# Optimization experiments

Measured on AMD Instinct MI355X. Metric: run time of the kernel, lower is better.

## Reference

```python
import jax, jax.numpy as jnp
import numpy as np

T, B, I, H = 1200, 32, 512, 512


def setup_inputs() -> dict:
    key = jax.random.key(0)
    ks = jax.random.split(key, 10)
    s = 0.1
    x = jax.random.normal(ks[0], (T, B, I), dtype=jnp.float32)
    lengths = jax.random.randint(ks[1], (B,), 1, T + 1)
    lengths = lengths.at[0].set(T)  # ensure padded output length == T (static shape)
    return {
        "x": x,
        "output_lengths": lengths,
        "w_ih_fwd": jax.random.normal(ks[2], (4 * H, I), dtype=jnp.float32) * s,
        "w_hh_fwd": jax.random.normal(ks[3], (4 * H, H), dtype=jnp.float32) * s,
        "b_ih_fwd": jax.random.normal(ks[4], (4 * H,), dtype=jnp.float32) * s,
        "b_hh_fwd": jax.random.normal(ks[5], (4 * H,), dtype=jnp.float32) * s,
        "w_ih_bwd": jax.random.normal(ks[6], (4 * H, I), dtype=jnp.float32) * s,
        "w_hh_bwd": jax.random.normal(ks[7], (4 * H, H), dtype=jnp.float32) * s,
        "b_ih_bwd": jax.random.normal(ks[8], (4 * H,), dtype=jnp.float32) * s,
        "b_hh_bwd": jax.random.normal(ks[9], (4 * H,), dtype=jnp.float32) * s,
    }


def _lstm_dir(x, mask, w_ih, w_hh, b_ih, b_hh):
    """Masked unidirectional LSTM (PyTorch gate order i,f,g,o).
    x: (T,B,I), mask: (T,B,1) bool. Returns outputs (T,B,H), (h_n, c_n)."""
    h0 = jnp.zeros((x.shape[1], w_hh.shape[1]), dtype=x.dtype)
    c0 = jnp.zeros_like(h0)
    # Precompute input projection for all timesteps at once (one big GEMM).
    x_proj = jnp.einsum('tbi,gi->tbg', x, w_ih) + (b_ih + b_hh)

    def step(carry, inp):
        h, c = carry
        xp, m = inp  # xp: (B,4H), m: (B,1)
        gates = xp + h @ w_hh.T
        i, f, g, o = jnp.split(gates, 4, axis=-1)
        i = jax.nn.sigmoid(i)
        f = jax.nn.sigmoid(f)
        g = jnp.tanh(g)
        o = jax.nn.sigmoid(o)
        c_new = f * c + i * g
        h_new = o * jnp.tanh(c_new)
        # Packed semantics: state frozen past each sequence's length.
        h = jnp.where(m, h_new, h)
        c = jnp.where(m, c_new, c)
        out = jnp.where(m, h_new, jnp.zeros_like(h_new))  # pad positions -> 0
        return (h, c), out

    (h_n, c_n), outs = jax.lax.scan(step, (h0, c0), (x_proj, mask))
    return outs, h_n, c_n


def reference(x, output_lengths, w_ih_fwd, w_hh_fwd, b_ih_fwd, b_hh_fwd,
              w_ih_bwd, w_hh_bwd, b_ih_bwd, b_hh_bwd):
    t_idx = jnp.arange(x.shape[0])  # (T,)
    mask = (t_idx[:, None] < output_lengths[None, :])[:, :, None]  # (T,B,1)

    # Forward direction.
    out_f, h_f, c_f = _lstm_dir(x, mask, w_ih_fwd, w_hh_fwd, b_ih_fwd, b_hh_fwd)

    # Backward direction: reverse each sequence within its valid region.
    rev_idx = jnp.clip(output_lengths[None, :] - 1 - t_idx[:, None], 0)  # (T,B)
    x_rev = jnp.take_along_axis(x, rev_idx[:, :, None], axis=0) * mask
    out_r, h_b, c_b = _lstm_dir(x_rev, mask, w_ih_bwd, w_hh_bwd, b_ih_bwd, b_hh_bwd)
    out_b = jnp.take_along_axis(out_r, rev_idx[:, :, None], axis=0) * mask

    # Bidirectional view(...,2,-1).sum(2) == sum of direction outputs.
    out = out_f + out_b
    h_n = jnp.stack([h_f, h_b], axis=0)  # (2,B,H)
    c_n = jnp.stack([c_f, c_b], axis=0)
    return out, h_n, c_n
```

## Files before the change

kernel.cpp:

```cpp
#include <hip/hip_runtime.h>
#include <cstdint>
#include <cstddef>

typedef unsigned short u16;
typedef unsigned int u32;
typedef unsigned long long u64;
typedef short bf16x8 __attribute__((ext_vector_type(8)));
typedef float f32x4 __attribute__((ext_vector_type(4)));
typedef unsigned short u16x4 __attribute__((ext_vector_type(4)));

#define T_LEN 1200

#define O_X     0ull
#define O_WIH   39321600ull
#define O_WHH   43515904ull
#define O_BIAS  47710208ull
#define O_HBUF  47726592ull
#define WS_NEED 47988736ull

#define HO 19660800ull
#define CO 19693568ull

#define HROW 516

__device__ __forceinline__ u16 f2bf(float f) {
  union { float f; unsigned u; } v; v.f = f;
  unsigned r = v.u + 0x7FFFu + ((v.u >> 16) & 1u);
  return (u16)(r >> 16);
}
__device__ __forceinline__ float sigm(float x) { return 1.f / (1.f + __expf(-x)); }
__device__ __forceinline__ float tanh_s(float x) {
  float ax = fabsf(x);
  float e = __expf(-2.f * ax);
  float t = (1.f - e) / (1.f + e);
  return x < 0.f ? -t : t;
}

__device__ __forceinline__ u64 ld_dev64(const u32* p) {
  return __hip_atomic_load((const u64*)p, __ATOMIC_RELAXED, __HIP_MEMORY_SCOPE_AGENT);
}
__device__ __forceinline__ u32 ld_dev32(const u32* p) {
  return __hip_atomic_load(p, __ATOMIC_RELAXED, __HIP_MEMORY_SCOPE_AGENT);
}
__device__ __forceinline__ void st_dev32(u32* p, unsigned v) {
  __hip_atomic_store(p, v, __ATOMIC_RELAXED, __HIP_MEMORY_SCOPE_AGENT);
}

__global__ __launch_bounds__(256) void cast_x_k(const float4* __restrict__ x,
                                                u16* __restrict__ xb) {
  int i = blockIdx.x * 256 + threadIdx.x;
  float4 v = x[i];
  u16x4 o;
  o.x = f2bf(v.x); o.y = f2bf(v.y); o.z = f2bf(v.z); o.w = f2bf(v.w);
  *(u16x4*)(xb + (size_t)i * 4) = o;
}

__global__ __launch_bounds__(256) void prep_w_k(
    const float* __restrict__ wih_f, const float* __restrict__ whh_f,
    const float* __restrict__ bih_f, const float* __restrict__ bhh_f,
    const float* __restrict__ wih_b, const float* __restrict__ whh_b,
    const float* __restrict__ bih_b, const float* __restrict__ bhh_b,
    u16* __restrict__ Wih, u16* __restrict__ Whh, float* __restrict__ bias) {
  int tid = blockIdx.x * 256 + threadIdx.x;
  int g = tid >> 9;
  float vi, vh;
  if (g < 2048) { vi = wih_f[tid]; vh = whh_f[tid]; }
  else { int t2 = tid - (2048 * 512); vi = wih_b[t2]; vh = whh_b[t2]; }
  Wih[tid] = f2bf(vi);
  Whh[tid] = f2bf(vh);
  if ((tid & 511) == 0) {
    bias[g] = (g < 2048) ? (bih_f[g] + bhh_f[g]) : (bih_b[g - 2048] + bhh_b[g - 2048]);
  }
}

__global__ __launch_bounds__(256, 1) void lstm_rec(const u16* __restrict__ X,
                                                   const u16* __restrict__ Wih,
                                                   const u16* __restrict__ Whh,
                                                   const float* __restrict__ bias,
                                                   const int* __restrict__ lengths,
                                                   u32* __restrict__ hbuf,
                                                   float* __restrict__ out) {
  const int tid = threadIdx.x, lane = tid & 63, wid = tid >> 6;
  const int bx = blockIdx.x;
  const int dir = bx >> 5, slice = bx & 31, c0 = slice * 16;
  const int quad = lane >> 4, l15 = lane & 15;

  __shared__ alignas(16) u16 h_l[32 * HROW];
  __shared__ float pre[4][32][16];
  __shared__ float s_out[8 * 512];
  __shared__ int len_s[32];

  if (tid < 32) len_s[tid] = lengths[tid];

  bf16x8 bh[16], bxw[16];
  {
    const size_t wrow = (size_t)(dir * 2048 + wid * 512 + c0 + l15) * 512 + quad * 8;
#pragma unroll
    for (int ks = 0; ks < 16; ++ks) {
      bh[ks]  = *(const bf16x8*)(Whh + wrow + (size_t)ks * 32);
      bxw[ks] = *(const bf16x8*)(Wih + wrow + (size_t)ks * 32);
    }
  }
  __syncthreads();

  const int b0 = tid >> 4, colv = tid & 15, b1 = b0 + 16;
  const int hcol = c0 + colv;
  const float bi  = bias[dir * 2048 + 0 * 512 + hcol];
  const float bfv = bias[dir * 2048 + 1 * 512 + hcol];
  const float bg  = bias[dir * 2048 + 2 * 512 + hcol];
  const float bo  = bias[dir * 2048 + 3 * 512 + hcol];

  float hreg0 = 0.f, hreg1 = 0.f, creg0 = 0.f, creg1 = 0.f;
  const int len0 = len_s[b0], len1 = len_s[b1];
  const int ba = l15, bb = 16 + l15;
  const int lena = len_s[ba], lenb = len_s[bb];

  bf16x8 ax0[16], ax1[16];
  {
    int tta = (dir == 0) ? 0 : (lena - 1);  if (tta < 0) tta = 0;
    int ttb = (dir == 0) ? 0 : (lenb - 1);  if (ttb < 0) ttb = 0;
    const u16* xrow0 = X + ((size_t)tta * 32 + ba) * 512 + quad * 8;
    const u16* xrow1 = X + ((size_t)ttb * 32 + bb) * 512 + quad * 8;
#pragma unroll
    for (int ks = 0; ks < 16; ++ks) {
      ax0[ks] = *(const bf16x8*)(xrow0 + (size_t)ks * 32);
      ax1[ks] = *(const bf16x8*)(xrow1 + (size_t)ks * 32);
    }
  }

  for (int t = 0; t < T_LEN; ++t) {
    u32* cur = hbuf + (size_t)(((t & 1) * 2 + dir) * 16384);
    u32* nxt = hbuf + (size_t)((((t + 1) & 1) * 2 + dir) * 16384);

    u64 stg[32];
#pragma unroll
    for (int j = 0; j < 32; ++j)
      stg[j] = ld_dev64(cur + j * 512 + tid * 2);

    f32x4 a0x = {0.f,0.f,0.f,0.f}, a1x = {0.f,0.f,0.f,0.f};
#pragma unroll
    for (int ks = 0; ks < 16; ++ks) {
      a0x = __builtin_amdgcn_mfma_f32_16x16x32_bf16(ax0[ks], bxw[ks], a0x, 0, 0, 0);
      a1x = __builtin_amdgcn_mfma_f32_16x16x32_bf16(ax1[ks], bxw[ks], a1x, 0, 0, 0);
    }

    const u64 e2 = ((u64)(u32)t << 32) | (u32)t;
    {
      u64 bad = 0;
#pragma unroll
      for (int j = 0; j < 32; ++j) bad |= (stg[j] ^ e2);
      if ((bad & 0x0000FFFF0000FFFFull) != 0) {
        const u32* sent = cur + 31 * 512 + (lane & 31) * 16;
        const u32 texp = (u32)t & 0xFFFFu;
        for (;;) {
          u32 v = ld_dev32(sent);
          if (__all((int)((v & 0xFFFFu) == texp))) break;
        }
        for (;;) {
#pragma unroll
          for (int j = 0; j < 32; ++j)
            stg[j] = ld_dev64(cur + j * 512 + tid * 2);
          bad = 0;
#pragma unroll
          for (int j = 0; j < 32; ++j) bad |= (stg[j] ^ e2);
          if ((bad & 0x0000FFFF0000FFFFull) == 0) break;
        }
      }
    }

    {
      int tn = t + 1;
      int tta = (dir == 0) ? (tn < T_LEN ? tn : T_LEN - 1) : (lena - 1 - tn);
      int ttb = (dir == 0) ? (tn < T_LEN ? tn : T_LEN - 1) : (lenb - 1 - tn);
      if (tta < 0) tta = 0;
      if (ttb < 0) ttb = 0;
      const u16* xrow0 = X + ((size_t)tta * 32 + ba) * 512 + quad * 8;
      const u16* xrow1 = X + ((size_t)ttb * 32 + bb) * 512 + quad * 8;
#pragma unroll
      for (int ks = 0; ks < 16; ++ks) {
        ax0[ks] = *(const bf16x8*)(xrow0 + (size_t)ks * 32);
        ax1[ks] = *(const bf16x8*)(xrow1 + (size_t)ks * 32);
      }
    }

#pragma unroll
    for (int j = 0; j < 32; ++j) {
      u32 d0 = (u32)stg[j], d1 = (u32)(stg[j] >> 32);
      *(u32*)&h_l[j * HROW + tid * 2] = (d0 >> 16) | (d1 & 0xFFFF0000u);
    }
    __syncthreads();

    f32x4 a0h = {0.f,0.f,0.f,0.f}, a1h = {0.f,0.f,0.f,0.f};
    const u16* hl0 = h_l + (size_t)l15 * HROW + quad * 8;
    const u16* hl1 = h_l + (size_t)(16 + l15) * HROW + quad * 8;
#pragma unroll
    for (int ks = 0; ks < 16; ++ks) {
      bf16x8 f0 = *(const bf16x8*)(hl0 + ks * 32);
      bf16x8 f1 = *(const bf16x8*)(hl1 + ks * 32);
      a0h = __builtin_amdgcn_mfma_f32_16x16x32_bf16(f0, bh[ks], a0h, 0, 0, 0);
      a1h = __builtin_amdgcn_mfma_f32_16x16x32_bf16(f1, bh[ks], a1h, 0, 0, 0);
    }
    f32x4 acc0 = a0x + a0h, acc1 = a1x + a1h;
#pragma unroll
    for (int r = 0; r < 4; ++r) {
      pre[wid][quad * 4 + r][l15]      = acc0[r];
      pre[wid][16 + quad * 4 + r][l15] = acc1[r];
    }
    __syncthreads();

    float hn0 = 0.f, hn1 = 0.f;
    if (t < len0) {
      float gi = pre[0][b0][colv] + bi,  gf = pre[1][b0][colv] + bfv;
      float gg = pre[2][b0][colv] + bg,  go = pre[3][b0][colv] + bo;
      float cn = sigm(gf) * creg0 + sigm(gi) * tanh_s(gg);
      hn0 = sigm(go) * tanh_s(cn);
      creg0 = cn; hreg0 = hn0;
    }
    if (t < len1) {
      float gi = pre[0][b1][colv] + bi,  gf = pre[1][b1][colv] + bfv;
      float gg = pre[2][b1][colv] + bg,  go = pre[3][b1][colv] + bo;
      float cn = sigm(gf) * creg1 + sigm(gi) * tanh_s(gg);
      hn1 = sigm(go) * tanh_s(cn);
      creg1 = cn; hreg1 = hn1;
    }

    const u32 tag = (u32)(t + 1);
    st_dev32(nxt + (size_t)b0 * 512 + hcol, ((u32)f2bf(hreg0) << 16) | tag);
    st_dev32(nxt + (size_t)b1 * 512 + hcol, ((u32)f2bf(hreg1) << 16) | tag);

    s_out[(t & 7) * 512 + tid]       = hn0;
    s_out[(t & 7) * 512 + 256 + tid] = hn1;
    if ((t & 7) == 7) {
#pragma unroll
      for (int k = 0; k < 8; ++k) {
        int ts = t - 7 + k;
        if (ts < len0) {
          int tt = (dir == 0) ? ts : (len0 - 1 - ts);
          atomicAdd(out + (size_t)(tt * 32 + b0) * 512 + hcol, s_out[k * 512 + tid]);
        }
        if (ts < len1) {
          int tt = (dir == 0) ? ts : (len1 - 1 - ts);
          atomicAdd(out + (size_t)(tt * 32 + b1) * 512 + hcol, s_out[k * 512 + 256 + tid]);
        }
      }
    }
  }

  out[HO + (size_t)dir * 16384 + (size_t)b0 * 512 + hcol] = hreg0;
  out[HO + (size_t)dir * 16384 + (size_t)b1 * 512 + hcol] = hreg1;
  out[CO + (size_t)dir * 16384 + (size_t)b0 * 512 + hcol] = creg0;
  out[CO + (size_t)dir * 16384 + (size_t)b1 * 512 + hcol] = creg1;
}

extern "C" void kernel_launch(void* const* d_in, const int* in_sizes, int n_in,
                              void* d_out, int out_size, void* d_ws, size_t ws_size,
                              hipStream_t stream) {
  const float* x     = (const float*)d_in[0];
  const int*   lens  = (const int*)d_in[1];
  const float* wih_f = (const float*)d_in[2];
  const float* whh_f = (const float*)d_in[3];
  const float* bih_f = (const float*)d_in[4];
  const float* bhh_f = (const float*)d_in[5];
  const float* wih_b = (const float*)d_in[6];
  const float* whh_b = (const float*)d_in[7];
  const float* bih_b = (const float*)d_in[8];
  const float* bhh_b = (const float*)d_in[9];
  float* out = (float*)d_out;
  char* ws = (char*)d_ws;

  u16*   xb   = (u16*)(ws + O_X);
  u16*   Wih  = (u16*)(ws + O_WIH);
  u16*   Whh  = (u16*)(ws + O_WHH);
  float* bias = (float*)(ws + O_BIAS);
  u32*   hbuf = (u32*)(ws + O_HBUF);

  hipMemsetAsync(hbuf, 0, 262144, stream);
  hipMemsetAsync(d_out, 0, (size_t)out_size * 4, stream);

  cast_x_k<<<19200, 256, 0, stream>>>((const float4*)x, xb);
  prep_w_k<<<8192, 256, 0, stream>>>(wih_f, whh_f, bih_f, bhh_f,
                                     wih_b, whh_b, bih_b, bhh_b, Wih, Whh, bias);
  lstm_rec<<<64, 256, 0, stream>>>(xb, Wih, Whh, bias, lens, hbuf, out);
}
```

Before: 11.53 ms.

## Co-locate each LSTM direction on one XCC and sync via XCC-local L2

Launches 256 blocks and uses the hardware XCC id plus atomic counters so the first 32 blocks landing on an XCC claim one direction, and the rest exit. A 24 KB LDS pad limits residency so blocks spread across XCCs. The hidden-state exchange then goes through XCC-local (sc0) loads and stores on a separate buffer instead of device-scope atomics, which is meant to cut the per-timestep cross-XCC synchronisation latency. A spin-count timeout falls back to the agent-scope buffer, which is still written every step. This relies on placement and inline-asm cache semantics and risks deadlock or slow fallback if the scheduler does not place 32 blocks per XCC.

```diff
diff --git a/kernel.cpp b/kernel.cpp
--- a/kernel.cpp
+++ b/kernel.cpp
@@ -16,12 +16,15 @@
 #define O_WHH   43515904ull
 #define O_BIAS  47710208ull
 #define O_HBUF  47726592ull
-#define WS_NEED 47988736ull
+#define O_XBUF  47988736ull
+#define O_CTL   48250880ull
+#define WS_NEED 48251392ull
 
 #define HO 19660800ull
 #define CO 19693568ull
 
 #define HROW 516
+#define TAGM 0x0000FFFF0000FFFFull
 
 __device__ __forceinline__ u16 f2bf(float f) {
   union { float f; unsigned u; } v; v.f = f;
@@ -38,9 +41,6 @@
 
 __device__ __forceinline__ u64 ld_dev64(const u32* p) {
   return __hip_atomic_load((const u64*)p, __ATOMIC_RELAXED, __HIP_MEMORY_SCOPE_AGENT);
-}
-__device__ __forceinline__ u32 ld_dev32(const u32* p) {
-  return __hip_atomic_load(p, __ATOMIC_RELAXED, __HIP_MEMORY_SCOPE_AGENT);
 }
 __device__ __forceinline__ void st_dev32(u32* p, unsigned v) {
   __hip_atomic_store(p, v, __ATOMIC_RELAXED, __HIP_MEMORY_SCOPE_AGENT);
@@ -79,18 +79,55 @@
                                                    const float* __restrict__ bias,
                                                    const int* __restrict__ lengths,
                                                    u32* __restrict__ hbuf,
-                                                   float* __restrict__ out) {
+                                                   u32* __restrict__ xbuf,
+                                                   float* __restrict__ out,
+                                                   int* __restrict__ ctl) {
   const int tid = threadIdx.x, lane = tid & 63, wid = tid >> 6;
-  const int bx = blockIdx.x;
-  const int dir = bx >> 5, slice = bx & 31, c0 = slice * 16;
   const int quad = lane >> 4, l15 = lane & 15;
 
   __shared__ alignas(16) u16 h_l[32 * HROW];
   __shared__ float pre[4][32][16];
   __shared__ float s_out[8 * 512];
   __shared__ int len_s[32];
+  __shared__ int s_dir, s_slice, s_slow;
+  __shared__ char lds_pad[24576];
 
   if (tid < 32) len_s[tid] = lengths[tid];
+  ((volatile char*)lds_pad)[tid] = 0;
+
+  if (tid == 0) {
+    int xcc;
+    asm volatile("s_getreg_b32 %0, hwreg(HW_REG_XCC_ID)" : "=s"(xcc));
+    xcc &= 7;
+    int slot = __hip_atomic_fetch_add(&ctl[xcc], 1, __ATOMIC_RELAXED,
+                                      __HIP_MEMORY_SCOPE_AGENT);
+    int mydir;
+    if (slot == 0) {
+      int d = __hip_atomic_fetch_add(&ctl[16], 1, __ATOMIC_RELAXED,
+                                     __HIP_MEMORY_SCOPE_AGENT);
+      mydir = (d < 2) ? d : 2;
+      __hip_atomic_store(&ctl[8 + xcc], mydir + 1, __ATOMIC_RELAXED,
+                         __HIP_MEMORY_SCOPE_AGENT);
+    } else if (slot < 32) {
+      int v;
+      do {
+        v = __hip_atomic_load(&ctl[8 + xcc], __ATOMIC_RELAXED,
+                              __HIP_MEMORY_SCOPE_AGENT);
+        if (v == 0) __builtin_amdgcn_s_sleep(2);
+      } while (v == 0);
+      mydir = v - 1;
+    } else {
+      mydir = 3;
+    }
+    s_dir = mydir;
+    s_slice = (slot < 32) ? slot : 0;
+    s_slow = 0;
+  }
+  __syncthreads();
+
+  if (s_dir >= 2) return;
+
+  const int dir = s_dir, slice = s_slice, c0 = slice * 16;
 
   bf16x8 bh[16], bxw[16];
   {
@@ -101,7 +138,6 @@
       bxw[ks] = *(const bf16x8*)(Wih + wrow + (size_t)ks * 32);
     }
   }
-  __syncthreads();
 
   const int b0 = tid >> 4, colv = tid & 15, b1 = b0 + 16;
   const int hcol = c0 + colv;
@@ -129,13 +165,24 @@
   }
 
   for (int t = 0; t < T_LEN; ++t) {
-    u32* cur = hbuf + (size_t)(((t & 1) * 2 + dir) * 16384);
-    u32* nxt = hbuf + (size_t)((((t + 1) & 1) * 2 + dir) * 16384);
+    const size_t boff = (size_t)(((t & 1) * 2 + dir) * 16384);
+    const size_t noff = (size_t)((((t + 1) & 1) * 2 + dir) * 16384);
+    const u32* xcur = xbuf + boff;  u32* xnxt = xbuf + noff;
+    const u32* hcur = hbuf + boff;  u32* hnxt = hbuf + noff;
+
+    bool slow = (s_slow != 0);
 
     u64 stg[32];
-#pragma unroll
-    for (int j = 0; j < 32; ++j)
-      stg[j] = ld_dev64(cur + j * 512 + tid * 2);
+    if (!slow) {
+#pragma unroll
+      for (int j = 0; j < 32; ++j)
+        asm volatile("global_load_dwordx2 %0, %1, off sc0"
+                     : "=v"(stg[j]) : "v"(xcur + (size_t)j * 512 + tid * 2));
+    } else {
+#pragma unroll
+      for (int j = 0; j < 32; ++j)
+        stg[j] = ld_dev64(hcur + (size_t)j * 512 + tid * 2);
+    }
 
     f32x4 a0x = {0.f,0.f,0.f,0.f}, a1x = {0.f,0.f,0.f,0.f};
 #pragma unroll
@@ -143,27 +190,53 @@
       a0x = __builtin_amdgcn_mfma_f32_16x16x32_bf16(ax0[ks], bxw[ks], a0x, 0, 0, 0);
       a1x = __builtin_amdgcn_mfma_f32_16x16x32_bf16(ax1[ks], bxw[ks], a1x, 0, 0, 0);
     }
+    if (!slow) asm volatile("s_waitcnt vmcnt(0)" ::: "memory");
 
     const u64 e2 = ((u64)(u32)t << 32) | (u32)t;
     {
       u64 bad = 0;
 #pragma unroll
       for (int j = 0; j < 32; ++j) bad |= (stg[j] ^ e2);
-      if ((bad & 0x0000FFFF0000FFFFull) != 0) {
-        const u32* sent = cur + 31 * 512 + (lane & 31) * 16;
-        const u32 texp = (u32)t & 0xFFFFu;
-        for (;;) {
-          u32 v = ld_dev32(sent);
-          if (__all((int)((v & 0xFFFFu) == texp))) break;
+      if ((bad & TAGM) != 0) {
+        bool need_agent = slow;
+        if (!slow) {
+          const u32* sent = xcur + 31 * 512 + (lane & 31) * 16;
+          const u32 texp = (u32)t & 0xFFFFu;
+          int it = 0;
+          for (;;) {
+            u32 v;
+            asm volatile("global_load_dword %0, %1, off sc0\n\ts_waitcnt vmcnt(0)"
+                         : "=v"(v) : "v"(sent));
+            if (__all((int)((v & 0xFFFFu) == texp))) break;
+            if (++it > 4096) { need_agent = true; break; }
+          }
+          if (!need_agent) {
+            int it2 = 0;
+            for (;;) {
+#pragma unroll
+              for (int j = 0; j < 32; ++j)
+                asm volatile("global_load_dwordx2 %0, %1, off sc0"
+                             : "=v"(stg[j]) : "v"(xcur + (size_t)j * 512 + tid * 2));
+              asm volatile("s_waitcnt vmcnt(0)" ::: "memory");
+              bad = 0;
+#pragma unroll
+              for (int j = 0; j < 32; ++j) bad |= (stg[j] ^ e2);
+              if ((bad & TAGM) == 0) break;
+              if (++it2 > 64) { need_agent = true; break; }
+            }
+          }
+          if (need_agent) s_slow = 1;
         }
-        for (;;) {
-#pragma unroll
-          for (int j = 0; j < 32; ++j)
-            stg[j] = ld_dev64(cur + j * 512 + tid * 2);
-          bad = 0;
-#pragma unroll
-          for (int j = 0; j < 32; ++j) bad |= (stg[j] ^ e2);
-          if ((bad & 0x0000FFFF0000FFFFull) == 0) break;
+        if (need_agent) {
+          for (;;) {
+#pragma unroll
+            for (int j = 0; j < 32; ++j)
+              stg[j] = ld_dev64(hcur + (size_t)j * 512 + tid * 2);
+            bad = 0;
+#pragma unroll
+            for (int j = 0; j < 32; ++j) bad |= (stg[j] ^ e2);
+            if ((bad & TAGM) == 0) break;
+          }
         }
       }
     }
@@ -225,8 +298,14 @@
     }
 
     const u32 tag = (u32)(t + 1);
-    st_dev32(nxt + (size_t)b0 * 512 + hcol, ((u32)f2bf(hreg0) << 16) | tag);
-    st_dev32(nxt + (size_t)b1 * 512 + hcol, ((u32)f2bf(hreg1) << 16) | tag);
+    u32 w0 = ((u32)f2bf(hreg0) << 16) | tag;
+    u32 w1 = ((u32)f2bf(hreg1) << 16) | tag;
+    asm volatile("global_store_dword %0, %1, off sc0"
+                 :: "v"(xnxt + (size_t)b0 * 512 + hcol), "v"(w0) : "memory");
+    asm volatile("global_store_dword %0, %1, off sc0"
+                 :: "v"(xnxt + (size_t)b1 * 512 + hcol), "v"(w1) : "memory");
+    st_dev32(hnxt + (size_t)b0 * 512 + hcol, w0);
+    st_dev32(hnxt + (size_t)b1 * 512 + hcol, w1);
 
     s_out[(t & 7) * 512 + tid]       = hn0;
     s_out[(t & 7) * 512 + 256 + tid] = hn1;
@@ -273,12 +352,14 @@
   u16*   Whh  = (u16*)(ws + O_WHH);
   float* bias = (float*)(ws + O_BIAS);
   u32*   hbuf = (u32*)(ws + O_HBUF);
-
-  hipMemsetAsync(hbuf, 0, 262144, stream);
+  u32*   xbu  = (u32*)(ws + O_XBUF);
+  int*   ctl  = (int*)(ws + O_CTL);
+
+  hipMemsetAsync(hbuf, 0, 262144 * 2 + 512, stream);
   hipMemsetAsync(d_out, 0, (size_t)out_size * 4, stream);
 
   cast_x_k<<<19200, 256, 0, stream>>>((const float4*)x, xb);
   prep_w_k<<<8192, 256, 0, stream>>>(wih_f, whh_f, bih_f, bhh_f,
                                      wih_b, whh_b, bih_b, bhh_b, Wih, Whh, bias);
-  lstm_rec<<<64, 256, 0, stream>>>(xb, Wih, Whh, bias, lens, hbuf, out);
-}
+  lstm_rec<<<256, 256, 0, stream>>>(xb, Wih, Whh, bias, lens, hbuf, xbu, out, ctl);
+}
```

New measurement: 13.26 ms. 14.9% more time.
